# Kernel tuning notes

Measured on AMD Instinct MI355X. Metric: run time of the kernel, lower is better.

Reference implementation:

```python
import jax, jax.numpy as jnp
import numpy as np


def setup_inputs() -> dict:
    key = jax.random.key(0)
    k1, k2 = jax.random.split(key)
    B, L, T, H = 8, 12, 1024, 256
    h_blth = jax.random.normal(k1, (B, L, T, H), dtype=jnp.float32)
    attn_w = jax.random.normal(k2, (1, H), dtype=jnp.float32) * (1.0 / np.sqrt(H))
    attn_b = jnp.zeros((1,), dtype=jnp.float32)
    return {"h_blth": h_blth, "attn_w": attn_w, "attn_b": attn_b}


def reference(h_blth, attn_w, attn_b):
    # s = Linear(H -> 1)(h).squeeze(-1): [B, L, T]
    s = jnp.einsum('blth,oh->blt', h_blth, attn_w) + attn_b[0]
    # global (non-causal) max over time axis, as in the original code
    s_max = jnp.max(s, axis=2, keepdims=True)
    exp_s = jnp.exp(s - s_max)                      # [B, L, T]
    cum_exp = jnp.cumsum(exp_s, axis=2)             # [B, L, T]
    weighted_h = exp_s[..., None] * h_blth          # [B, L, T, H]
    cum_weighted_h = jnp.cumsum(weighted_h, axis=2) # [B, L, T, H]
    ctx = cum_weighted_h / (cum_exp[..., None] + 1e-12)
    return h_blth + ctx
```

## Files before the change

### kernel.cpp

```cpp
#include <hip/hip_runtime.h>

#define RWS 96
#define TT  1024
#define HH  256
#define CT  64
#define NC  (TT/CT)

typedef float f32x4 __attribute__((ext_vector_type(4)));

__global__ __launch_bounds__(256) void ta_pass1(
    const float* __restrict__ h, const float* __restrict__ attn_w,
    const float* __restrict__ attn_b, float* __restrict__ e_g,
    float* __restrict__ W_g) {
  const int blk  = blockIdx.x;
  const int row  = blk / NC;
  const int c    = blk % NC;
  const int t0   = c * CT;
  const int tid  = threadIdx.x;
  const int lane = tid & 63;
  const int wave = tid >> 6;

  const float4 wv  = reinterpret_cast<const float4*>(attn_w)[lane];
  const float bias = attn_b[0];
  const float* hrow = h + (size_t)row * TT * HH;

  float4 acc = make_float4(0.f, 0.f, 0.f, 0.f);

  for (int tt = wave; tt < CT; tt += 4) {
    const int t = t0 + tt;
    const float4 hv =
        reinterpret_cast<const float4*>(hrow + (size_t)t * HH)[lane];
    float p = hv.x * wv.x + hv.y * wv.y + hv.z * wv.z + hv.w * wv.w;
#pragma unroll
    for (int off = 32; off; off >>= 1) p += __shfl_xor(p, off);
    const float e = __expf(p + bias);
    if (lane == 0) e_g[(size_t)row * TT + t] = e;
    acc.x = fmaf(e, hv.x, acc.x);
    acc.y = fmaf(e, hv.y, acc.y);
    acc.z = fmaf(e, hv.z, acc.z);
    acc.w = fmaf(e, hv.w, acc.w);
  }

  __shared__ float wlds[4][HH];
  reinterpret_cast<float4*>(wlds[wave])[lane] = acc;
  __syncthreads();
  const float wsum = wlds[0][tid] + wlds[1][tid] + wlds[2][tid] + wlds[3][tid];
  W_g[((size_t)row * NC + c) * HH + tid] = wsum;
}

__global__ __launch_bounds__(64) void ta_pass2(
    const float* __restrict__ h, const float* __restrict__ e_g,
    const float* __restrict__ W_g, float* __restrict__ out) {
  const int blk  = blockIdx.x;
  const int row  = blk >> 4;
  const int c    = blk & (NC - 1);
  const int ts   = c * CT;
  const int lane = threadIdx.x;

  const float* er = e_g + (size_t)row * TT;
  const float ev = er[ts + lane];

  float ex = 0.f;
  for (int i = lane; i < ts; i += 64) ex += er[i];
#pragma unroll
  for (int off = 32; off; off >>= 1) ex += __shfl_xor(ex, off);

  float4 run = make_float4(0.f, 0.f, 0.f, 0.f);
  const float4* Wp =
      reinterpret_cast<const float4*>(W_g + (size_t)row * NC * HH) + lane;
  for (int cc = 0; cc < c; ++cc) {
    const float4 wv = Wp[(size_t)cc * (HH / 4)];
    run.x += wv.x; run.y += wv.y; run.z += wv.z; run.w += wv.w;
  }

  const f32x4* hp =
      reinterpret_cast<const f32x4*>(h + ((size_t)row * TT + ts) * HH) + lane;
  f32x4* op =
      reinterpret_cast<f32x4*>(out + ((size_t)row * TT + ts) * HH) + lane;

  float cum = ex;
#pragma unroll 8
  for (int tt = 0; tt < CT; ++tt) {
    const float e = __shfl(ev, tt);
    cum += e;
    const float ic = __builtin_amdgcn_rcpf(cum + 1e-12f);
    const f32x4 hv = __builtin_nontemporal_load(hp + (size_t)tt * (HH / 4));
    run.x = fmaf(e, hv.x, run.x);
    run.y = fmaf(e, hv.y, run.y);
    run.z = fmaf(e, hv.z, run.z);
    run.w = fmaf(e, hv.w, run.w);
    f32x4 o;
    o.x = fmaf(run.x, ic, hv.x);
    o.y = fmaf(run.y, ic, hv.y);
    o.z = fmaf(run.z, ic, hv.z);
    o.w = fmaf(run.w, ic, hv.w);
    __builtin_nontemporal_store(o, op + (size_t)tt * (HH / 4));
  }
}

extern "C" void kernel_launch(void* const* d_in, const int* in_sizes, int n_in,
                              void* d_out, int out_size, void* d_ws,
                              size_t ws_size, hipStream_t stream) {
  const float* h      = (const float*)d_in[0];
  const float* attn_w = (const float*)d_in[1];
  const float* attn_b = (const float*)d_in[2];
  float* out = (float*)d_out;

  float* e_g = (float*)d_ws;
  float* W_g = e_g + (size_t)RWS * TT;

  ta_pass1<<<RWS * NC, 256, 0, stream>>>(h, attn_w, attn_b, e_g, W_g);
  ta_pass2<<<RWS * NC, 64, 0, stream>>>(h, e_g, W_g, out);
}
```

Before: 56.71 us.

## Split pass-2 chunks into four 16-step wave segments with per-wave prefix sums

Pass 1 now assigns each wave a contiguous 16-step segment and writes per-segment weighted sums (W16) alongside the per-chunk totals. Pass 2 runs four waves per block, so each wave scans only 16 timesteps after combining chunk and sub-chunk prefixes, which shortens the serial scan chain per wave. The exp values are staged in shared memory for reuse. Nontemporal loads and stores are replaced with ordinary ones. The cost is extra W16 workspace traffic and extra prefix reads in pass 2.

```diff
diff --git a/kernel.cpp b/kernel.cpp
--- a/kernel.cpp
+++ b/kernel.cpp
@@ -5,13 +5,14 @@
 #define HH  256
 #define CT  64
 #define NC  (TT/CT)
+#define NG  (TT/16)
 
 typedef float f32x4 __attribute__((ext_vector_type(4)));
 
 __global__ __launch_bounds__(256) void ta_pass1(
     const float* __restrict__ h, const float* __restrict__ attn_w,
     const float* __restrict__ attn_b, float* __restrict__ e_g,
-    float* __restrict__ W_g) {
+    float* __restrict__ W16, float* __restrict__ Wc) {
   const int blk  = blockIdx.x;
   const int row  = blk / NC;
   const int c    = blk % NC;
@@ -20,16 +21,18 @@
   const int lane = tid & 63;
   const int wave = tid >> 6;
 
-  const float4 wv  = reinterpret_cast<const float4*>(attn_w)[lane];
+  const f32x4 wv   = reinterpret_cast<const f32x4*>(attn_w)[lane];
   const float bias = attn_b[0];
   const float* hrow = h + (size_t)row * TT * HH;
+  const int tw = t0 + wave * 16;
 
-  float4 acc = make_float4(0.f, 0.f, 0.f, 0.f);
+  f32x4 acc = {0.f, 0.f, 0.f, 0.f};
 
-  for (int tt = wave; tt < CT; tt += 4) {
-    const int t = t0 + tt;
-    const float4 hv =
-        reinterpret_cast<const float4*>(hrow + (size_t)t * HH)[lane];
+#pragma unroll 4
+  for (int i = 0; i < 16; ++i) {
+    const int t = tw + i;
+    const f32x4 hv =
+        reinterpret_cast<const f32x4*>(hrow + (size_t)t * HH)[lane];
     float p = hv.x * wv.x + hv.y * wv.y + hv.z * wv.z + hv.w * wv.w;
 #pragma unroll
     for (int off = 32; off; off >>= 1) p += __shfl_xor(p, off);
@@ -41,50 +44,66 @@
     acc.w = fmaf(e, hv.w, acc.w);
   }
 
+  reinterpret_cast<f32x4*>(W16 + ((size_t)row * NG + c * 4 + wave) * HH)[lane] =
+      acc;
+
   __shared__ float wlds[4][HH];
-  reinterpret_cast<float4*>(wlds[wave])[lane] = acc;
+  reinterpret_cast<f32x4*>(wlds[wave])[lane] = acc;
   __syncthreads();
-  const float wsum = wlds[0][tid] + wlds[1][tid] + wlds[2][tid] + wlds[3][tid];
-  W_g[((size_t)row * NC + c) * HH + tid] = wsum;
+  const float s = wlds[0][tid] + wlds[1][tid] + wlds[2][tid] + wlds[3][tid];
+  Wc[((size_t)row * NC + c) * HH + tid] = s;
 }
 
-__global__ __launch_bounds__(64) void ta_pass2(
+__global__ __launch_bounds__(256) void ta_pass2(
     const float* __restrict__ h, const float* __restrict__ e_g,
-    const float* __restrict__ W_g, float* __restrict__ out) {
+    const float* __restrict__ W16, const float* __restrict__ Wc,
+    float* __restrict__ out) {
   const int blk  = blockIdx.x;
   const int row  = blk >> 4;
   const int c    = blk & (NC - 1);
   const int ts   = c * CT;
-  const int lane = threadIdx.x;
+  const int tid  = threadIdx.x;
+  const int lane = tid & 63;
+  const int wave = tid >> 6;
 
-  const float* er = e_g + (size_t)row * TT;
-  const float ev = er[ts + lane];
+  __shared__ float e_lds[TT];
+  reinterpret_cast<f32x4*>(e_lds)[tid] =
+      reinterpret_cast<const f32x4*>(e_g + (size_t)row * TT)[tid];
+  __syncthreads();
+
+  const int tsw = ts + wave * 16;
 
   float ex = 0.f;
-  for (int i = lane; i < ts; i += 64) ex += er[i];
+  for (int i = lane; i < tsw; i += 64) ex += e_lds[i];
 #pragma unroll
   for (int off = 32; off; off >>= 1) ex += __shfl_xor(ex, off);
 
-  float4 run = make_float4(0.f, 0.f, 0.f, 0.f);
-  const float4* Wp =
-      reinterpret_cast<const float4*>(W_g + (size_t)row * NC * HH) + lane;
+  f32x4 run = {0.f, 0.f, 0.f, 0.f};
+  const f32x4* Wcp =
+      reinterpret_cast<const f32x4*>(Wc + (size_t)row * NC * HH) + lane;
   for (int cc = 0; cc < c; ++cc) {
-    const float4 wv = Wp[(size_t)cc * (HH / 4)];
+    const f32x4 wv = Wcp[(size_t)cc * (HH / 4)];
+    run.x += wv.x; run.y += wv.y; run.z += wv.z; run.w += wv.w;
+  }
+  const f32x4* Wgp =
+      reinterpret_cast<const f32x4*>(W16 + ((size_t)row * NG + c * 4) * HH) +
+      lane;
+  for (int g = 0; g < wave; ++g) {
+    const f32x4 wv = Wgp[(size_t)g * (HH / 4)];
     run.x += wv.x; run.y += wv.y; run.z += wv.z; run.w += wv.w;
   }
 
   const f32x4* hp =
-      reinterpret_cast<const f32x4*>(h + ((size_t)row * TT + ts) * HH) + lane;
+      reinterpret_cast<const f32x4*>(h + ((size_t)row * TT + tsw) * HH) + lane;
   f32x4* op =
-      reinterpret_cast<f32x4*>(out + ((size_t)row * TT + ts) * HH) + lane;
-
+      reinterpret_cast<f32x4*>(out + ((size_t)row * TT + tsw) * HH) + lane;
   float cum = ex;
-#pragma unroll 8
-  for (int tt = 0; tt < CT; ++tt) {
-    const float e = __shfl(ev, tt);
+#pragma unroll 4
+  for (int i = 0; i < 16; ++i) {
+    const float e = e_lds[tsw + i];
     cum += e;
     const float ic = __builtin_amdgcn_rcpf(cum + 1e-12f);
-    const f32x4 hv = __builtin_nontemporal_load(hp + (size_t)tt * (HH / 4));
+    const f32x4 hv = hp[(size_t)i * (HH / 4)];
     run.x = fmaf(e, hv.x, run.x);
     run.y = fmaf(e, hv.y, run.y);
     run.z = fmaf(e, hv.z, run.z);
@@ -94,7 +113,7 @@
     o.y = fmaf(run.y, ic, hv.y);
     o.z = fmaf(run.z, ic, hv.z);
     o.w = fmaf(run.w, ic, hv.w);
-    __builtin_nontemporal_store(o, op + (size_t)tt * (HH / 4));
+    op[(size_t)i * (HH / 4)] = o;
   }
 }
 
@@ -107,8 +126,9 @@
   float* out = (float*)d_out;
 
   float* e_g = (float*)d_ws;
-  float* W_g = e_g + (size_t)RWS * TT;
+  float* W16 = e_g + (size_t)RWS * TT;
+  float* Wc  = W16 + (size_t)RWS * NG * HH;
 
-  ta_pass1<<<RWS * NC, 256, 0, stream>>>(h, attn_w, attn_b, e_g, W_g);
-  ta_pass2<<<RWS * NC, 64, 0, stream>>>(h, e_g, W_g, out);
+  ta_pass1<<<RWS * NC, 256, 0, stream>>>(h, attn_w, attn_b, e_g, W16, Wc);
+  ta_pass2<<<RWS * NC, 256, 0, stream>>>(h, e_g, W16, Wc, out);
 }
```

Result: no change. 56.71 us (+0.0%).
